# Kernel tuning notes

Measured on AMD Instinct MI355X. Metric: run time of the kernel, lower is better.

The kernel has to match this reference:

```python
import jax, jax.numpy as jnp
import numpy as np

B_, L, D_MODEL = 8, 2048, 512
EXPAND, D_STATE, HEADDIM, NGROUPS, D_CONV = 2, 16, 64, 1, 4
D_INNER = EXPAND * D_MODEL            # 1024
NHEADS = D_INNER // HEADDIM           # 16
CONV_DIM = D_INNER + 2 * NGROUPS * D_STATE   # 1056
D_IN_PROJ = 2 * D_INNER + 2 * NGROUPS * D_STATE + NHEADS  # 2096
EPS = 1e-5


def _mamba_params(key):
    ks = jax.random.split(key, 5)
    in_proj_w = jax.random.normal(ks[0], (D_IN_PROJ, D_MODEL), jnp.float32) * (D_MODEL ** -0.5)
    conv_w = jax.random.normal(ks[1], (CONV_DIM, 1, D_CONV), jnp.float32) * (D_CONV ** -0.5)
    conv_b = jnp.zeros((CONV_DIM,), jnp.float32)
    # inverse-softplus of dt ~ U[1e-3, 0.1] (mamba-ssm style init)
    dt_bias = jnp.log(jnp.expm1(jax.random.uniform(ks[2], (NHEADS,), jnp.float32, 1e-3, 0.1)))
    A_log = jnp.log(jax.random.uniform(ks[3], (NHEADS,), jnp.float32, 1.0, 16.0))
    Dp = jnp.ones((NHEADS,), jnp.float32)
    norm_w = jnp.ones((D_INNER,), jnp.float32)
    out_proj_w = jax.random.normal(ks[4], (D_MODEL, D_INNER), jnp.float32) * (D_INNER ** -0.5)
    return [in_proj_w, conv_w, conv_b, dt_bias, A_log, Dp, norm_w, out_proj_w]


def setup_inputs() -> dict:
    key = jax.random.key(0)
    k0, k1, k2 = jax.random.split(key, 3)
    d = {"x": jax.random.normal(k0, (B_, L, D_MODEL), jnp.float32)}
    names = ["in_proj_w", "conv_w", "conv_b", "dt_bias", "A_log", "Dp", "norm_w", "out_proj_w"]
    for pre, k in (("fwd_", k1), ("bwd_", k2)):
        for n, p in zip(names, _mamba_params(k)):
            d[pre + n] = p
    return d


def _silu(v):
    return v * jax.nn.sigmoid(v)


def _mamba2(u, in_proj_w, conv_w, conv_b, dt_bias, A_log, Dp, norm_w, out_proj_w):
    b, l, _ = u.shape
    zxbcdt = u @ in_proj_w.T                                # (b,l,D_IN_PROJ)
    z, xBC, dt = jnp.split(zxbcdt, [D_INNER, D_INNER + CONV_DIM], axis=-1)
    # causal depthwise conv1d + silu
    xc = jnp.transpose(xBC, (0, 2, 1))                      # (b,C,l)
    xc = jax.lax.conv_general_dilated(xc, conv_w, (1,), [(D_CONV - 1, 0)],
                                      feature_group_count=CONV_DIM)
    xBC = _silu(jnp.transpose(xc, (0, 2, 1)) + conv_b)      # (b,l,C)
    xs, Bm, Cm = jnp.split(xBC, [D_INNER, D_INNER + NGROUPS * D_STATE], axis=-1)
    xs = xs.reshape(b, l, NHEADS, HEADDIM)
    Bm = Bm.reshape(b, l, NGROUPS, D_STATE)[:, :, 0]        # ngroups=1 -> (b,l,N)
    Cm = Cm.reshape(b, l, NGROUPS, D_STATE)[:, :, 0]
    dt = jax.nn.softplus(dt + dt_bias)                      # (b,l,H)
    A = -jnp.exp(A_log)                                     # (H,)
    dA = jnp.exp(dt * A)                                    # (b,l,H), in (0,1)

    def step(h, inp):
        dA_t, dt_t, x_t, B_t, C_t = inp
        h = h * dA_t[:, :, None, None] + jnp.einsum('bh,bhp,bn->bhpn', dt_t, x_t, B_t)
        y = jnp.einsum('bhpn,bn->bhp', h, C_t)
        return h, y

    h0 = jnp.zeros((b, NHEADS, HEADDIM, D_STATE), u.dtype)
    seq = (jnp.moveaxis(dA, 1, 0), jnp.moveaxis(dt, 1, 0), jnp.moveaxis(xs, 1, 0),
           jnp.moveaxis(Bm, 1, 0), jnp.moveaxis(Cm, 1, 0))
    _, ys = jax.lax.scan(step, h0, seq)
    y = jnp.moveaxis(ys, 0, 1) + xs * Dp[None, None, :, None]   # (b,l,H,P)
    y = y.reshape(b, l, D_INNER)
    # RMSNormGated (norm_before_gate=False): rmsnorm(y * silu(z)) * w
    y = y * _silu(z)
    y = y * jax.lax.rsqrt(jnp.mean(y * y, axis=-1, keepdims=True) + EPS) * norm_w
    return y @ out_proj_w.T


def reference(x,
              fwd_in_proj_w, fwd_conv_w, fwd_conv_b, fwd_dt_bias, fwd_A_log, fwd_Dp, fwd_norm_w, fwd_out_proj_w,
              bwd_in_proj_w, bwd_conv_w, bwd_conv_b, bwd_dt_bias, bwd_A_log, bwd_Dp, bwd_norm_w, bwd_out_proj_w):
    fwd = _mamba2(x, fwd_in_proj_w, fwd_conv_w, fwd_conv_b, fwd_dt_bias, fwd_A_log, fwd_Dp, fwd_norm_w, fwd_out_proj_w)
    bwd = _mamba2(x[:, ::-1], bwd_in_proj_w, bwd_conv_w, bwd_conv_b, bwd_dt_bias, bwd_A_log, bwd_Dp, bwd_norm_w, bwd_out_proj_w)
    return fwd + bwd[:, ::-1]
```

## Files before the change

kernel.cpp:

```cpp
#include <hip/hip_runtime.h>
#include <stdint.h>

#define L_SEQ   2048
#define BATCH   8
#define DMODEL  512
#define DINNER  1024
#define NHEADS  16
#define HEADDIM 64
#define DSTATE  16
#define CONVDIM 1056
#define DINPROJ 2096
#define NPROJ   4192
#define NPROJ_P 4224
#define NROWS   (BATCH*L_SEQ)
#define NCH     32
#define CHLEN   64
#define XBCW    1072

typedef __attribute__((ext_vector_type(8))) short short8;
typedef __attribute__((ext_vector_type(4))) float f32x4;

static __device__ __forceinline__ unsigned short f2bf(float f) {
    unsigned int u = __float_as_uint(f);
    u += 0x7FFF + ((u >> 16) & 1);
    return (unsigned short)(u >> 16);
}
static __device__ __forceinline__ float bf2f(unsigned short u) {
    return __uint_as_float((unsigned int)u << 16);
}
static __device__ __forceinline__ float silu(float v) {
    return v / (1.f + __expf(-v));
}
static __device__ __forceinline__ void glds16(const unsigned short* g, unsigned short* l) {
    __builtin_amdgcn_global_load_lds(
        (const __attribute__((address_space(1))) unsigned int*)g,
        (__attribute__((address_space(3))) unsigned int*)l, 16, 0, 0);
}

#define PREP_N1 (NROWS*DMODEL)
#define PREP_N2 (NPROJ_P*DMODEL)
#define PREP_N3 (512*2048)
#define PREP_T  ((PREP_N1+PREP_N2+PREP_N3)/4)
static __device__ __forceinline__ uint2 pack4(float4 v) {
    uint2 o;
    o.x = (unsigned int)f2bf(v.x) | ((unsigned int)f2bf(v.y) << 16);
    o.y = (unsigned int)f2bf(v.z) | ((unsigned int)f2bf(v.w) << 16);
    return o;
}
__global__ void k_prep(const float* __restrict__ x,
                       const float* __restrict__ fwi, const float* __restrict__ bwi,
                       const float* __restrict__ fow, const float* __restrict__ bow,
                       unsigned short* __restrict__ XB, unsigned short* __restrict__ W1,
                       unsigned short* __restrict__ W2) {
    int i = blockIdx.x * 256 + threadIdx.x;
    if (i >= PREP_T) return;
    int j4 = i * 4;
    if (j4 < PREP_N1) {
        *(uint2*)&XB[j4] = pack4(*(const float4*)&x[j4]);
    } else if (j4 < PREP_N1 + PREP_N2) {
        int j = j4 - PREP_N1;
        const int FS = DINPROJ * DMODEL;
        uint2 o = {0u, 0u};
        if (j < 2 * FS)
            o = pack4(j < FS ? *(const float4*)&fwi[j] : *(const float4*)&bwi[j - FS]);
        *(uint2*)&W1[j] = o;
    } else {
        int j = j4 - PREP_N1 - PREP_N2;
        int n = j >> 11, k = j & 2047;
        const float* s = (k < DINNER) ? &fow[n * DINNER + k] : &bow[n * DINNER + k - DINNER];
        *(uint2*)&W2[j] = pack4(*(const float4*)s);
    }
}

#define BM 128
#define BN 128
#define BK 32

#define GEMM_BODY(NROUNDS, EPILOGUE)                                                        \
    __shared__ __align__(16) unsigned short as[2][BM][BK];                                  \
    __shared__ __align__(16) unsigned short bs[2][BN][BK];                                  \
    const int tid = threadIdx.x;                                                            \
    const int lane = tid & 63;                                                              \
    const int wave = tid >> 6;                                                              \
    const int wm = (wave & 1) * 64;                                                         \
    const int wn = (wave >> 1) * 64;                                                        \
    const int l16 = lane & 15;                                                              \
    const int q = lane >> 4;                                                                \
    const int sr = wave * 32;                                                               \
    const int lr = lane >> 2;                                                               \
    const int lc = (lane & 3) * 8;                                                          \
    f32x4 acc[4][4];                                                                        \
    for (int i = 0; i < 4; i++)                                                             \
        for (int j = 0; j < 4; j++) acc[i][j] = (f32x4){0.f, 0.f, 0.f, 0.f};                \
    const unsigned short* Ab = A + (size_t)(bm + sr + lr) * K + koff + lc;                  \
    const unsigned short* Bb = Bw + (size_t)(bn + sr + lr) * K + koff + lc;                 \
    glds16(Ab, &as[0][sr][0]);                                                              \
    glds16(Ab + (size_t)16 * K, &as[0][sr + 16][0]);                                        \
    glds16(Bb, &bs[0][sr][0]);                                                              \
    glds16(Bb + (size_t)16 * K, &bs[0][sr + 16][0]);                                        \
    __syncthreads();                                                                        \
    for (int r = 0; r < NROUNDS; r++) {                                                     \
        const int pb = r & 1;                                                               \
        if (r + 1 < NROUNDS) {               \
            const int kb = (r + 1) * BK;                                                    \
            glds16(Ab + kb, &as[pb ^ 1][sr][0]);                                            \
            glds16(Ab + (size_t)16 * K + kb, &as[pb ^ 1][sr + 16][0]);                      \
            glds16(Bb + kb, &bs[pb ^ 1][sr][0]);                                            \
            glds16(Bb + (size_t)16 * K + kb, &bs[pb ^ 1][sr + 16][0]);                      \
        }                                                                                   \
        short8 af[4], bfr[4];                                                               \
        for (int i = 0; i < 4; i++) af[i] = *(const short8*)&as[pb][wm + i * 16 + l16][q * 8]; \
        for (int j = 0; j < 4; j++) bfr[j] = *(const short8*)&bs[pb][wn + j * 16 + l16][q * 8]; \
        for (int i = 0; i < 4; i++)                                                         \
            for (int j = 0; j < 4; j++)                                                     \
                acc[i][j] = __builtin_amdgcn_mfma_f32_16x16x32_bf16(af[i], bfr[j], acc[i][j], 0, 0, 0); \
        __syncthreads();                          \
    }                                                                                       \
    EPILOGUE

#define GEMM_BODY_OUT(NROUNDS, EPILOGUE)                                                    \
    __shared__ __align__(16) unsigned short as[2][64][BK];                                  \
    __shared__ __align__(16) unsigned short bs[2][BN][BK];                                  \
    const int tid = threadIdx.x;                                                            \
    const int lane = tid & 63;                                                              \
    const int wave = tid >> 6;                                                              \
    const int wm = (wave & 1) * 32;                                                         \
    const int wn = (wave >> 1) * 64;                                                        \
    const int l16 = lane & 15;                                                              \
    const int q = lane >> 4;                                                                \
    const int sra = wave * 16;                                                              \
    const int srb = wave * 32;                                                              \
    const int lr = lane >> 2;                                                               \
    const int lc = (lane & 3) * 8;                                                          \
    f32x4 acc[2][4];                                                                        \
    for (int i = 0; i < 2; i++)                                                             \
        for (int j = 0; j < 4; j++) acc[i][j] = (f32x4){0.f, 0.f, 0.f, 0.f};                \
    const unsigned short* Ab = A + (size_t)(bm + sra + lr) * K + koff + lc;                 \
    const unsigned short* Bb = Bw + (size_t)(bn + srb + lr) * K + koff + lc;                \
    glds16(Ab, &as[0][sra][0]);                                                             \
    glds16(Bb, &bs[0][srb][0]);                                                             \
    glds16(Bb + (size_t)16 * K, &bs[0][srb + 16][0]);                                       \
    __syncthreads();                                                                        \
    for (int r = 0; r < NROUNDS; r++) {                                                     \
        const int pb = r & 1;                                                               \
        if (r + 1 < NROUNDS) {                                                              \
            const int kb = (r + 1) * BK;                                                    \
            glds16(Ab + kb, &as[pb ^ 1][sra][0]);                                           \
            glds16(Bb + kb, &bs[pb ^ 1][srb][0]);                                           \
            glds16(Bb + (size_t)16 * K + kb, &bs[pb ^ 1][srb + 16][0]);                     \
        }                                                                                   \
        short8 af[2], bfr[4];                                                               \
        for (int i = 0; i < 2; i++) af[i] = *(const short8*)&as[pb][wm + i * 16 + l16][q * 8]; \
        for (int j = 0; j < 4; j++) bfr[j] = *(const short8*)&bs[pb][wn + j * 16 + l16][q * 8]; \
        for (int i = 0; i < 2; i++)                                                         \
            for (int j = 0; j < 4; j++)                                                     \
                acc[i][j] = __builtin_amdgcn_mfma_f32_16x16x32_bf16(af[i], bfr[j], acc[i][j], 0, 0, 0); \
        __syncthreads();                                                                    \
    }                                                                                       \
    EPILOGUE

__global__ __launch_bounds__(256, 4) void k_gemm_proj(const unsigned short* __restrict__ A,
                                                      const unsigned short* __restrict__ Bw,
                                                      unsigned short* __restrict__ ZG,
                                                      unsigned short* __restrict__ XBCDT) {
    const int K = DMODEL;
    const int N = NPROJ;
    const int lin = blockIdx.x;
    const int xcd = lin & 7;
    const int idx = lin >> 3;
    const int mloc = idx & 15;
    const int n_tile = idx >> 4;
    const int bm = (mloc * 8 + xcd) * BM;
    const int bn = n_tile * BN;
    const int koff = 0;
    GEMM_BODY(16, {
        for (int i = 0; i < 4; i++) {
            int row0 = bm + wm + i * 16 + q * 4;
            for (int j = 0; j < 4; j++) {
                int col = bn + wn + j * 16 + l16;
                if (col < N) {
                    int dir = col >= DINPROJ;
                    int cc = col - dir * DINPROJ;
                    for (int r = 0; r < 4; r++) {
                        unsigned short v = f2bf(acc[i][j][r]);
                        size_t rowo = (size_t)(dir * NROWS + row0 + r);
                        if (cc < DINNER)
                            ZG[rowo * DINNER + cc] = v;
                        else
                            XBCDT[rowo * XBCW + (cc - DINNER)] = v;
                    }
                }
            }
        }
    })
}

__global__ __launch_bounds__(256) void k_gemm_out(const unsigned short* __restrict__ A,
                                                  const unsigned short* __restrict__ Bw,
                                                  float* __restrict__ C) {
    const int K = 2048;
    const int lin = blockIdx.x;
    const int xcd = lin & 7;
    const int idx = lin >> 3;
    const int mloc = idx & 31;
    const int n_tile = idx >> 5;
    const int bm = (mloc * 8 + xcd) * 64;
    const int bn = n_tile * BN;
    const int koff = 0;
    GEMM_BODY_OUT(64, {
        for (int i = 0; i < 2; i++) {
            int row0 = bm + wm + i * 16 + q * 4;
            for (int j = 0; j < 4; j++) {
                int col = bn + wn + j * 16 + l16;
                for (int r = 0; r < 4; r++)
                    C[(size_t)(row0 + r) * 512 + col] = acc[i][j][r];
            }
        }
    })
}

__global__ __launch_bounds__(256) void k_conv2(const unsigned short* __restrict__ XBCDT,
                                               const float* __restrict__ fw_w, const float* __restrict__ fw_b,
                                               const float* __restrict__ bw_w, const float* __restrict__ bw_b,
                                               unsigned short* __restrict__ XS, float* __restrict__ BCb) {
    __shared__ unsigned short sm[70][256];
    int t = threadIdx.x;
    int bidx = blockIdx.x;
    int lcn = bidx & 31;
    int b   = (bidx >> 5) & 7;
    int dir = (bidx >> 8) & 1;
    int ct  = bidx >> 9;
    int c0 = ct * 256;
    int l0 = lcn * 64;
    int c = c0 + t;
    const unsigned short* src = XBCDT + (size_t)dir * NROWS * XBCW;
    {
        const int rr = t >> 5;
        const int ch = t & 31;
        const int cc0 = c0 + ch * 8;
        const bool cok16 = (cc0 + 8 <= XBCW);
        const short8 z8 = {0, 0, 0, 0, 0, 0, 0, 0};
#pragma unroll
        for (int pass = 0; pass < 9; ++pass) {
            int r = pass * 8 + rr;
            if (r < 70) {
                int li = l0 - 3 + r;
                short8 v = z8;
                if (li >= 0 && li < L_SEQ && cok16)
                    v = *(const short8*)&src[(size_t)((b << 11) + li) * XBCW + cc0];
                *(short8*)&sm[r][ch * 8] = v;
            }
        }
    }
    __syncthreads();
    if (c >= CONVDIM) return;
    const float* w = (dir ? bw_w : fw_w) + c * 4;
    float bias = (dir ? bw_b : fw_b)[c];
    float wr[4];
    if (dir) { wr[0] = w[3]; wr[1] = w[2]; wr[2] = w[1]; wr[3] = w[0]; }
    else     { wr[0] = w[0]; wr[1] = w[1]; wr[2] = w[2]; wr[3] = w[3]; }
    int o = dir ? 3 : 0;
    float w0 = bf2f(sm[o][t]), w1 = bf2f(sm[o + 1][t]), w2 = bf2f(sm[o + 2][t]);
    unsigned short* xso = XS + (size_t)dir * NROWS * DINNER;
    float* bco = BCb + (size_t)dir * NROWS * 32;
    int rowbase = (b << 11) + l0;
#pragma unroll 4
    for (int l = 0; l < 64; l++) {
        float w3 = bf2f(sm[l + o + 3][t]);
        float acc = ((wr[0] * w0 + wr[1] * w1) + (wr[2] * w2 + wr[3] * w3)) + bias;
        float v = silu(acc);
        int row = rowbase + l;
        if (c < DINNER)
            xso[(size_t)row * DINNER + c] = f2bf(v);
        else
            bco[(size_t)row * 32 + (c - DINNER)] = v;
        w0 = w1; w1 = w2; w2 = w3;
    }
}

__global__ void k_dt(const unsigned short* __restrict__ XBCDT,
                     const float* __restrict__ fdtb, const float* __restrict__ fAl,
                     const float* __restrict__ bdtb, const float* __restrict__ bAl,
                     float* __restrict__ DT, float* __restrict__ DA) {
    int gid = blockIdx.x * 256 + threadIdx.x;
    if (gid >= 2 * NROWS * NHEADS) return;
    int h = gid & 15;
    int row = (gid >> 4) & (NROWS - 1);
    int dir = gid >> 18;
    float dtb = (dir ? bdtb : fdtb)[h];
    float Al = (dir ? bAl : fAl)[h];
    float x = bf2f(XBCDT[(size_t)(dir * NROWS + row) * XBCW + CONVDIM + h]) + dtb;
    float dt = (x > 15.f) ? x : log1pf(__expf(x));
    float dA = __expf(-__expf(Al) * dt);
    DT[gid] = dt;
    DA[gid] = dA;
}

__global__ __launch_bounds__(64) void k_scan_state(const unsigned short* __restrict__ XS,
                                                   const float* __restrict__ BCb,
                                                   const float* __restrict__ DT,
                                                   const float* __restrict__ DA,
                                                   float* __restrict__ S, float* __restrict__ P) {
    int idx = blockIdx.x;
    int c = idx & 31, hp = (idx >> 5) & 7, b = (idx >> 8) & 7, dir = idx >> 11;
    int t = threadIdx.x;
    int h = hp * 2 + (t >> 5);
    int p0 = (t & 31) * 2;
    const unsigned short* xs = XS + (size_t)dir * NROWS * DINNER;
    const float* bc = BCb + (size_t)dir * NROWS * 32;
    const float* dtp = DT + (size_t)dir * NROWS * NHEADS;
    const float* dap = DA + (size_t)dir * NROWS * NHEADS;
    float hreg0[16], hreg1[16];
#pragma unroll
    for (int n = 0; n < 16; n++) { hreg0[n] = 0.f; hreg1[n] = 0.f; }
    float Pp = 1.f;
#pragma unroll 4
    for (int tl = 0; tl < CHLEN; ++tl) {
        int tt = c * CHLEN + tl;
        int l = dir ? (L_SEQ - 1 - tt) : tt;
        int row = (b << 11) + l;
        unsigned int xv2 = *(const unsigned int*)&xs[(size_t)row * DINNER + h * HEADDIM + p0];
        float xv0 = bf2f((unsigned short)(xv2 & 0xffff));
        float xv1 = bf2f((unsigned short)(xv2 >> 16));
        float dt = dtp[row * 16 + h];
        float dA = dap[row * 16 + h];
        f32x4 Bv[4];
#pragma unroll
        for (int qq = 0; qq < 4; qq++) Bv[qq] = *(const f32x4*)&bc[(size_t)row * 32 + qq * 4];
        float k0 = dt * xv0, k1 = dt * xv1;
#pragma unroll
        for (int n = 0; n < 16; n++) {
            float bv = Bv[n >> 2][n & 3];
            hreg0[n] = fmaf(hreg0[n], dA, k0 * bv);
            hreg1[n] = fmaf(hreg1[n], dA, k1 * bv);
        }
        Pp *= dA;
    }
    int sh = (((dir * 8 + b) * 16 + h) * NCH + c);
#pragma unroll
    for (int qq = 0; qq < 4; qq++) {
        f32x4 v0 = {hreg0[qq * 4], hreg0[qq * 4 + 1], hreg0[qq * 4 + 2], hreg0[qq * 4 + 3]};
        f32x4 v1 = {hreg1[qq * 4], hreg1[qq * 4 + 1], hreg1[qq * 4 + 2], hreg1[qq * 4 + 3]};
        *(f32x4*)&S[(size_t)sh * 1024 + p0 * 16 + qq * 4] = v0;
        *(f32x4*)&S[(size_t)sh * 1024 + (p0 + 1) * 16 + qq * 4] = v1;
    }
    if ((t & 31) == 0) P[sh] = Pp;
}

__global__ void k_combine(float* __restrict__ S, const float* __restrict__ P,
                          float* __restrict__ SSQ) {
    int gid = blockIdx.x * 256 + threadIdx.x;
    if (gid < 2 * NROWS) SSQ[gid] = 0.f;
    if (gid >= 2 * 8 * 16 * 1024) return;
    int pn = gid & 1023;
    int base = gid >> 10;
    float H = 0.f;
#pragma unroll 4
    for (int c = 0; c < NCH; c++) {
        size_t o = ((size_t)base * NCH + c) * 1024 + pn;
        float s = S[o];
        S[o] = H;
        H = H * P[base * NCH + c] + s;
    }
}

__global__ __launch_bounds__(64) void k_scan_out(const unsigned short* __restrict__ XS,
                                                 const float* __restrict__ BCb,
                                                 const float* __restrict__ DT,
                                                 const float* __restrict__ DA,
                                                 const float* __restrict__ Hinit,
                                                 const float* __restrict__ fDp,
                                                 const float* __restrict__ bDp,
                                                 const unsigned short* __restrict__ ZG,
                                                 float* __restrict__ SSQ,
                                                 unsigned short* __restrict__ Y) {
    int idx = blockIdx.x;
    int c = idx & 31, hp = (idx >> 5) & 7, b = (idx >> 8) & 7, dir = idx >> 11;
    int t = threadIdx.x;
    int h = hp * 2 + (t >> 5);
    int p0 = (t & 31) * 2;
    const unsigned short* xs = XS + (size_t)dir * NROWS * DINNER;
    const unsigned short* zgd = ZG + (size_t)dir * NROWS * DINNER;
    const float* bc = BCb + (size_t)dir * NROWS * 32;
    const float* dtp = DT + (size_t)dir * NROWS * NHEADS;
    const float* dap = DA + (size_t)dir * NROWS * NHEADS;
    unsigned short* yo = Y + (size_t)dir * NROWS * DINNER;
    float* ssqd = SSQ + (size_t)dir * NROWS;
    float Dpv = (dir ? bDp : fDp)[h];
    int sh = (((dir * 8 + b) * 16 + h) * NCH + c);
    float hreg0[16], hreg1[16];
#pragma unroll
    for (int qq = 0; qq < 4; qq++) {
        f32x4 v0 = *(const f32x4*)&Hinit[(size_t)sh * 1024 + p0 * 16 + qq * 4];
        f32x4 v1 = *(const f32x4*)&Hinit[(size_t)sh * 1024 + (p0 + 1) * 16 + qq * 4];
#pragma unroll
        for (int e = 0; e < 4; e++) { hreg0[qq * 4 + e] = v0[e]; hreg1[qq * 4 + e] = v1[e]; }
    }
#pragma unroll 4
    for (int tl = 0; tl < CHLEN; ++tl) {
        int tt = c * CHLEN + tl;
        int l = dir ? (L_SEQ - 1 - tt) : tt;
        int row = (b << 11) + l;
        unsigned int xv2 = *(const unsigned int*)&xs[(size_t)row * DINNER + h * HEADDIM + p0];
        float xv0 = bf2f((unsigned short)(xv2 & 0xffff));
        float xv1 = bf2f((unsigned short)(xv2 >> 16));
        float dt = dtp[row * 16 + h];
        float dA = dap[row * 16 + h];
        f32x4 Bv[4], Cv[4];
#pragma unroll
        for (int qq = 0; qq < 4; qq++) Bv[qq] = *(const f32x4*)&bc[(size_t)row * 32 + qq * 4];
#pragma unroll
        for (int qq = 0; qq < 4; qq++) Cv[qq] = *(const f32x4*)&bc[(size_t)row * 32 + 16 + qq * 4];
        float k0 = dt * xv0, k1 = dt * xv1;
        float y0 = 0.f, y1 = 0.f;
#pragma unroll
        for (int n = 0; n < 16; n++) {
            float bv = Bv[n >> 2][n & 3];
            float cv = Cv[n >> 2][n & 3];
            hreg0[n] = fmaf(hreg0[n], dA, k0 * bv);
            hreg1[n] = fmaf(hreg1[n], dA, k1 * bv);
            y0 = fmaf(hreg0[n], cv, y0);
            y1 = fmaf(hreg1[n], cv, y1);
        }
        unsigned int zz = *(const unsigned int*)&zgd[(size_t)row * DINNER + h * HEADDIM + p0];
        float v0 = (y0 + xv0 * Dpv) * silu(bf2f((unsigned short)(zz & 0xffff)));
        float v1 = (y1 + xv1 * Dpv) * silu(bf2f((unsigned short)(zz >> 16)));
        unsigned int yw = (unsigned int)f2bf(v0) | ((unsigned int)f2bf(v1) << 16);
        *(unsigned int*)&yo[(size_t)row * DINNER + h * HEADDIM + p0] = yw;
        float pr = v0 * v0 + v1 * v1;
#pragma unroll
        for (int off = 16; off > 0; off >>= 1) pr += __shfl_down(pr, off);
        if ((t & 31) == 0) atomicAdd(&ssqd[row], pr);
    }
}

__global__ __launch_bounds__(256) void k_gatenorm(const unsigned short* __restrict__ Y,
                                                  const float* __restrict__ SSQ,
                                                  const float* __restrict__ fnw,
                                                  const float* __restrict__ bnw,
                                                  unsigned short* __restrict__ NRM) {
    int bid = blockIdx.x;
    int t = threadIdx.x;
    int sub = t >> 7;
    int tt = t & 127;
    int rid = bid * 2 + sub;
    int dir = rid >> 14;
    int row = rid & (NROWS - 1);
    int c = tt * 8;
    const size_t base = (size_t)rid * DINNER + c;
    uint4 yu = *(const uint4*)&Y[base];
    float scale = rsqrtf(SSQ[rid] * (1.f / 1024.f) + 1e-5f);
    const float* nw = (dir ? bnw : fnw) + c;
    f32x4 nw0 = *(const f32x4*)&nw[0];
    f32x4 nw1 = *(const f32x4*)&nw[4];
    const unsigned int yw[4] = {yu.x, yu.y, yu.z, yu.w};
    unsigned int ow[4];
#pragma unroll
    for (int e = 0; e < 4; e++) {
        float a = bf2f((unsigned short)(yw[e] & 0xffff)) * scale
                * (e < 2 ? nw0[e * 2]     : nw1[(e - 2) * 2]);
        float b = bf2f((unsigned short)(yw[e] >> 16)) * scale
                * (e < 2 ? nw0[e * 2 + 1] : nw1[(e - 2) * 2 + 1]);
        ow[e] = (unsigned int)f2bf(a) | ((unsigned int)f2bf(b) << 16);
    }
    uint4 o = {ow[0], ow[1], ow[2], ow[3]};
    *(uint4*)&NRM[(size_t)row * 2048 + dir * DINNER + c] = o;
}

extern "C" void kernel_launch(void* const* d_in, const int* in_sizes, int n_in,
                              void* d_out, int out_size, void* d_ws, size_t ws_size,
                              hipStream_t stream) {
    const float* x     = (const float*)d_in[0];
    const float* f_inw = (const float*)d_in[1];
    const float* f_cw  = (const float*)d_in[2];
    const float* f_cb  = (const float*)d_in[3];
    const float* f_dtb = (const float*)d_in[4];
    const float* f_Al  = (const float*)d_in[5];
    const float* f_Dp  = (const float*)d_in[6];
    const float* f_nw  = (const float*)d_in[7];
    const float* f_ow  = (const float*)d_in[8];
    const float* b_inw = (const float*)d_in[9];
    const float* b_cw  = (const float*)d_in[10];
    const float* b_cb  = (const float*)d_in[11];
    const float* b_dtb = (const float*)d_in[12];
    const float* b_Al  = (const float*)d_in[13];
    const float* b_Dp  = (const float*)d_in[14];
    const float* b_nw  = (const float*)d_in[15];
    const float* b_ow  = (const float*)d_in[16];

    char* ws = (char*)d_ws;
    size_t off = 0;
    auto alloc = [&](size_t bytes) {
        void* p = ws + off;
        off += (bytes + 255) & ~(size_t)255;
        return p;
    };
    unsigned short* XBCDT = (unsigned short*)alloc((size_t)2 * NROWS * XBCW * 2);
    unsigned short* NRM   = XBCDT;
    float* S = (float*)XBCDT;
    float* P = (float*)((char*)XBCDT + (size_t)2 * 8 * 16 * NCH * 1024 * 4);
    unsigned short* XS    = (unsigned short*)alloc((size_t)2 * NROWS * DINNER * 2);
    unsigned short* Yb    = XS;
    unsigned short* ZG    = (unsigned short*)alloc((size_t)2 * NROWS * DINNER * 2);
    unsigned short* W2    = (unsigned short*)alloc((size_t)512 * 2048 * 2);
    float* BCb  = (float*)alloc((size_t)2 * NROWS * 32 * 4);
    float* DT   = (float*)alloc((size_t)2 * NROWS * NHEADS * 4);
    float* DA   = (float*)alloc((size_t)2 * NROWS * NHEADS * 4);
    float* SSQ  = (float*)alloc((size_t)2 * NROWS * 4);
    char* unionBase = (char*)alloc((size_t)16777216 + (size_t)NPROJ_P * DMODEL * 2);
    unsigned short* XB = (unsigned short*)unionBase;
    unsigned short* W1 = (unsigned short*)(unionBase + 16777216);

    if (ws_size < off) return;

    k_prep<<<(PREP_T + 255) / 256, 256, 0, stream>>>(x, f_inw, b_inw, f_ow, b_ow, XB, W1, W2);
    k_gemm_proj<<<8 * 16 * 33, 256, 0, stream>>>(XB, W1, ZG, XBCDT);
    k_conv2<<<5 * 2 * 8 * 32, 256, 0, stream>>>(XBCDT, f_cw, f_cb, b_cw, b_cb, XS, BCb);
    {
        int n = 2 * NROWS * NHEADS;
        k_dt<<<(n + 255) / 256, 256, 0, stream>>>(XBCDT, f_dtb, f_Al, b_dtb, b_Al, DT, DA);
    }
    k_scan_state<<<2 * 8 * 8 * NCH, 64, 0, stream>>>(XS, BCb, DT, DA, S, P);
    {
        int n = 2 * 8 * 16 * 1024;
        k_combine<<<(n + 255) / 256, 256, 0, stream>>>(S, P, SSQ);
    }
    k_scan_out<<<2 * 8 * 8 * NCH, 64, 0, stream>>>(XS, BCb, DT, DA, S, f_Dp, b_Dp, ZG, SSQ, Yb);
    k_gatenorm<<<NROWS, 256, 0, stream>>>(Yb, SSQ, f_nw, b_nw, NRM);
    k_gemm_out<<<8 * 32 * 4, 256, 0, stream>>>(NRM, W2, (float*)d_out);
}
```

Before: 479.5 us.

## Fuse gated RMSNorm into output GEMM via weight folding and epilogue scaling

Removes the separate gate-norm kernel. The norm weight is folded into the bf16 output projection weights during prep, and the per-row rsqrt scale is applied in the GEMM epilogue. Forward and backward halves go into separate accumulators so each can take its own row scale. This saves a full read and write pass over the normalized activation buffer, at the cost of extra accumulator registers in the output GEMM and a slightly different rounding order.

```diff
diff --git a/kernel.cpp b/kernel.cpp
--- a/kernel.cpp
+++ b/kernel.cpp
@@ -50,6 +50,7 @@
 __global__ void k_prep(const float* __restrict__ x,
                        const float* __restrict__ fwi, const float* __restrict__ bwi,
                        const float* __restrict__ fow, const float* __restrict__ bow,
+                       const float* __restrict__ fnw, const float* __restrict__ bnw,
                        unsigned short* __restrict__ XB, unsigned short* __restrict__ W1,
                        unsigned short* __restrict__ W2) {
     int i = blockIdx.x * 256 + threadIdx.x;
@@ -67,8 +68,12 @@
     } else {
         int j = j4 - PREP_N1 - PREP_N2;
         int n = j >> 11, k = j & 2047;
-        const float* s = (k < DINNER) ? &fow[n * DINNER + k] : &bow[n * DINNER + k - DINNER];
-        *(uint2*)&W2[j] = pack4(*(const float4*)s);
+        float4 wv = (k < DINNER) ? *(const float4*)&fow[n * DINNER + k]
+                                 : *(const float4*)&bow[n * DINNER + k - DINNER];
+        float4 nv = (k < DINNER) ? *(const float4*)&fnw[k]
+                                 : *(const float4*)&bnw[k - DINNER];
+        wv.x *= nv.x; wv.y *= nv.y; wv.z *= nv.z; wv.w *= nv.w;
+        *(uint2*)&W2[j] = pack4(wv);
     }
 }
 
@@ -118,47 +123,6 @@
     }                                                                                       \
     EPILOGUE
 
-#define GEMM_BODY_OUT(NROUNDS, EPILOGUE)                                                    \
-    __shared__ __align__(16) unsigned short as[2][64][BK];                                  \
-    __shared__ __align__(16) unsigned short bs[2][BN][BK];                                  \
-    const int tid = threadIdx.x;                                                            \
-    const int lane = tid & 63;                                                              \
-    const int wave = tid >> 6;                                                              \
-    const int wm = (wave & 1) * 32;                                                         \
-    const int wn = (wave >> 1) * 64;                                                        \
-    const int l16 = lane & 15;                                                              \
-    const int q = lane >> 4;                                                                \
-    const int sra = wave * 16;                                                              \
-    const int srb = wave * 32;                                                              \
-    const int lr = lane >> 2;                                                               \
-    const int lc = (lane & 3) * 8;                                                          \
-    f32x4 acc[2][4];                                                                        \
-    for (int i = 0; i < 2; i++)                                                             \
-        for (int j = 0; j < 4; j++) acc[i][j] = (f32x4){0.f, 0.f, 0.f, 0.f};                \
-    const unsigned short* Ab = A + (size_t)(bm + sra + lr) * K + koff + lc;                 \
-    const unsigned short* Bb = Bw + (size_t)(bn + srb + lr) * K + koff + lc;                \
-    glds16(Ab, &as[0][sra][0]);                                                             \
-    glds16(Bb, &bs[0][srb][0]);                                                             \
-    glds16(Bb + (size_t)16 * K, &bs[0][srb + 16][0]);                                       \
-    __syncthreads();                                                                        \
-    for (int r = 0; r < NROUNDS; r++) {                                                     \
-        const int pb = r & 1;                                                               \
-        if (r + 1 < NROUNDS) {                                                              \
-            const int kb = (r + 1) * BK;                                                    \
-            glds16(Ab + kb, &as[pb ^ 1][sra][0]);                                           \
-            glds16(Bb + kb, &bs[pb ^ 1][srb][0]);                                           \
-            glds16(Bb + (size_t)16 * K + kb, &bs[pb ^ 1][srb + 16][0]);                     \
-        }                                                                                   \
-        short8 af[2], bfr[4];                                                               \
-        for (int i = 0; i < 2; i++) af[i] = *(const short8*)&as[pb][wm + i * 16 + l16][q * 8]; \
-        for (int j = 0; j < 4; j++) bfr[j] = *(const short8*)&bs[pb][wn + j * 16 + l16][q * 8]; \
-        for (int i = 0; i < 2; i++)                                                         \
-            for (int j = 0; j < 4; j++)                                                     \
-                acc[i][j] = __builtin_amdgcn_mfma_f32_16x16x32_bf16(af[i], bfr[j], acc[i][j], 0, 0, 0); \
-        __syncthreads();                                                                    \
-    }                                                                                       \
-    EPILOGUE
-
 __global__ __launch_bounds__(256, 4) void k_gemm_proj(const unsigned short* __restrict__ A,
                                                       const unsigned short* __restrict__ Bw,
                                                       unsigned short* __restrict__ ZG,
@@ -195,10 +159,12 @@
     })
 }
 
-__global__ __launch_bounds__(256) void k_gemm_out(const unsigned short* __restrict__ A,
+__global__ __launch_bounds__(256) void k_gemm_out(const unsigned short* __restrict__ Y,
                                                   const unsigned short* __restrict__ Bw,
+                                                  const float* __restrict__ SSQ,
                                                   float* __restrict__ C) {
-    const int K = 2048;
+    __shared__ __align__(16) unsigned short as[2][64][BK];
+    __shared__ __align__(16) unsigned short bs[2][BN][BK];
     const int lin = blockIdx.x;
     const int xcd = lin & 7;
     const int idx = lin >> 3;
@@ -206,17 +172,67 @@
     const int n_tile = idx >> 5;
     const int bm = (mloc * 8 + xcd) * 64;
     const int bn = n_tile * BN;
-    const int koff = 0;
-    GEMM_BODY_OUT(64, {
-        for (int i = 0; i < 2; i++) {
-            int row0 = bm + wm + i * 16 + q * 4;
+    const int tid = threadIdx.x;
+    const int lane = tid & 63;
+    const int wave = tid >> 6;
+    const int wm = (wave & 1) * 32;
+    const int wn = (wave >> 1) * 64;
+    const int l16 = lane & 15;
+    const int q = lane >> 4;
+    const int sra = wave * 16;
+    const int srb = wave * 32;
+    const int lr = lane >> 2;
+    const int lc = (lane & 3) * 8;
+    f32x4 accA[2][4], accF[2][4];
+    for (int i = 0; i < 2; i++)
+        for (int j = 0; j < 4; j++) {
+            accA[i][j] = (f32x4){0.f, 0.f, 0.f, 0.f};
+            accF[i][j] = (f32x4){0.f, 0.f, 0.f, 0.f};
+        }
+    const unsigned short* AF = Y + (size_t)(bm + sra + lr) * DINNER + lc;
+    const unsigned short* AB = AF + (size_t)NROWS * DINNER;
+    const unsigned short* Bb = Bw + (size_t)(bn + srb + lr) * 2048 + lc;
+    glds16(AF, &as[0][sra][0]);
+    glds16(Bb, &bs[0][srb][0]);
+    glds16(Bb + (size_t)16 * 2048, &bs[0][srb + 16][0]);
+    __syncthreads();
+    for (int r = 0; r < 64; r++) {
+        const int pb = r & 1;
+        if (r + 1 < 64) {
+            const int t = r + 1;
+            const unsigned short* asrc = (t < 32) ? AF + t * BK : AB + (t - 32) * BK;
+            const int kb = t * BK;
+            glds16(asrc, &as[pb ^ 1][sra][0]);
+            glds16(Bb + kb, &bs[pb ^ 1][srb][0]);
+            glds16(Bb + (size_t)16 * 2048 + kb, &bs[pb ^ 1][srb + 16][0]);
+        }
+        if (r == 32) {
+            for (int i = 0; i < 2; i++)
+                for (int j = 0; j < 4; j++) {
+                    accF[i][j] = accA[i][j];
+                    accA[i][j] = (f32x4){0.f, 0.f, 0.f, 0.f};
+                }
+        }
+        short8 af[2], bfr[4];
+        for (int i = 0; i < 2; i++) af[i] = *(const short8*)&as[pb][wm + i * 16 + l16][q * 8];
+        for (int j = 0; j < 4; j++) bfr[j] = *(const short8*)&bs[pb][wn + j * 16 + l16][q * 8];
+        for (int i = 0; i < 2; i++)
+            for (int j = 0; j < 4; j++)
+                accA[i][j] = __builtin_amdgcn_mfma_f32_16x16x32_bf16(af[i], bfr[j], accA[i][j], 0, 0, 0);
+        __syncthreads();
+    }
+    for (int i = 0; i < 2; i++) {
+        int row0 = bm + wm + i * 16 + q * 4;
+        for (int r = 0; r < 4; r++) {
+            int row = row0 + r;
+            float sf = rsqrtf(SSQ[row] * (1.f / 1024.f) + 1e-5f);
+            float sb = rsqrtf(SSQ[NROWS + row] * (1.f / 1024.f) + 1e-5f);
             for (int j = 0; j < 4; j++) {
                 int col = bn + wn + j * 16 + l16;
-                for (int r = 0; r < 4; r++)
-                    C[(size_t)(row0 + r) * 512 + col] = acc[i][j][r];
+                C[(size_t)row * 512 + col] = sf * accF[i][j][r] + sb * accA[i][j][r];
             }
         }
-    })
+    }
 }
 
 __global__ __launch_bounds__(256) void k_conv2(const unsigned short* __restrict__ XBCDT,
@@ -434,39 +450,6 @@
     }
 }
 
-__global__ __launch_bounds__(256) void k_gatenorm(const unsigned short* __restrict__ Y,
-                                                  const float* __restrict__ SSQ,
-                                                  const float* __restrict__ fnw,
-                                                  const float* __restrict__ bnw,
-                                                  unsigned short* __restrict__ NRM) {
-    int bid = blockIdx.x;
-    int t = threadIdx.x;
-    int sub = t >> 7;
-    int tt = t & 127;
-    int rid = bid * 2 + sub;
-    int dir = rid >> 14;
-    int row = rid & (NROWS - 1);
-    int c = tt * 8;
-    const size_t base = (size_t)rid * DINNER + c;
-    uint4 yu = *(const uint4*)&Y[base];
-    float scale = rsqrtf(SSQ[rid] * (1.f / 1024.f) + 1e-5f);
-    const float* nw = (dir ? bnw : fnw) + c;
-    f32x4 nw0 = *(const f32x4*)&nw[0];
-    f32x4 nw1 = *(const f32x4*)&nw[4];
-    const unsigned int yw[4] = {yu.x, yu.y, yu.z, yu.w};
-    unsigned int ow[4];
-#pragma unroll
-    for (int e = 0; e < 4; e++) {
-        float a = bf2f((unsigned short)(yw[e] & 0xffff)) * scale
-                * (e < 2 ? nw0[e * 2]     : nw1[(e - 2) * 2]);
-        float b = bf2f((unsigned short)(yw[e] >> 16)) * scale
-                * (e < 2 ? nw0[e * 2 + 1] : nw1[(e - 2) * 2 + 1]);
-        ow[e] = (unsigned int)f2bf(a) | ((unsigned int)f2bf(b) << 16);
-    }
-    uint4 o = {ow[0], ow[1], ow[2], ow[3]};
-    *(uint4*)&NRM[(size_t)row * 2048 + dir * DINNER + c] = o;
-}
-
 extern "C" void kernel_launch(void* const* d_in, const int* in_sizes, int n_in,
                               void* d_out, int out_size, void* d_ws, size_t ws_size,
                               hipStream_t stream) {
@@ -496,7 +479,6 @@
         return p;
     };
     unsigned short* XBCDT = (unsigned short*)alloc((size_t)2 * NROWS * XBCW * 2);
-    unsigned short* NRM   = XBCDT;
     float* S = (float*)XBCDT;
     float* P = (float*)((char*)XBCDT + (size_t)2 * 8 * 16 * NCH * 1024 * 4);
     unsigned short* XS    = (unsigned short*)alloc((size_t)2 * NROWS * DINNER * 2);
@@ -513,7 +495,8 @@
 
     if (ws_size < off) return;
 
-    k_prep<<<(PREP_T + 255) / 256, 256, 0, stream>>>(x, f_inw, b_inw, f_ow, b_ow, XB, W1, W2);
+    k_prep<<<(PREP_T + 255) / 256, 256, 0, stream>>>(x, f_inw, b_inw, f_ow, b_ow,
+                                                     f_nw, b_nw, XB, W1, W2);
     k_gemm_proj<<<8 * 16 * 33, 256, 0, stream>>>(XB, W1, ZG, XBCDT);
     k_conv2<<<5 * 2 * 8 * 32, 256, 0, stream>>>(XBCDT, f_cw, f_cb, b_cw, b_cb, XS, BCb);
     {
@@ -526,6 +509,5 @@
         k_combine<<<(n + 255) / 256, 256, 0, stream>>>(S, P, SSQ);
     }
     k_scan_out<<<2 * 8 * 8 * NCH, 64, 0, stream>>>(XS, BCb, DT, DA, S, f_Dp, b_Dp, ZG, SSQ, Yb);
-    k_gatenorm<<<NROWS, 256, 0, stream>>>(Yb, SSQ, f_nw, b_nw, NRM);
-    k_gemm_out<<<8 * 32 * 4, 256, 0, stream>>>(NRM, W2, (float*)d_out);
-}
+    k_gemm_out<<<8 * 32 * 4, 256, 0, stream>>>(Yb, W2, SSQ, (float*)d_out);
+}
```

Result: no change. 483.2 us (+0.8%).

## Move gating and RMS sum-of-squares from scan into gatenorm block reduction

Applied to the files above, without the earlier changes.

The scan output kernel no longer reads the z gate, applies silu, or does per-row atomicAdd of squared values. It now writes the ungated y directly. The gatenorm kernel loads y and z, applies the gate, and computes the row sum of squares with a wave shuffle plus a shared-memory reduction. This removes atomic contention and the SSQ buffer and its zeroing, at the cost of an extra z read in gatenorm and one more bf16 rounding before gating.

```diff
diff --git a/kernel.cpp b/kernel.cpp
--- a/kernel.cpp
+++ b/kernel.cpp
@@ -347,10 +347,8 @@
     if ((t & 31) == 0) P[sh] = Pp;
 }
 
-__global__ void k_combine(float* __restrict__ S, const float* __restrict__ P,
-                          float* __restrict__ SSQ) {
+__global__ void k_combine(float* __restrict__ S, const float* __restrict__ P) {
     int gid = blockIdx.x * 256 + threadIdx.x;
-    if (gid < 2 * NROWS) SSQ[gid] = 0.f;
     if (gid >= 2 * 8 * 16 * 1024) return;
     int pn = gid & 1023;
     int base = gid >> 10;
@@ -371,8 +369,6 @@
                                                  const float* __restrict__ Hinit,
                                                  const float* __restrict__ fDp,
                                                  const float* __restrict__ bDp,
-                                                 const unsigned short* __restrict__ ZG,
-                                                 float* __restrict__ SSQ,
                                                  unsigned short* __restrict__ Y) {
     int idx = blockIdx.x;
     int c = idx & 31, hp = (idx >> 5) & 7, b = (idx >> 8) & 7, dir = idx >> 11;
@@ -380,12 +376,10 @@
     int h = hp * 2 + (t >> 5);
     int p0 = (t & 31) * 2;
     const unsigned short* xs = XS + (size_t)dir * NROWS * DINNER;
-    const unsigned short* zgd = ZG + (size_t)dir * NROWS * DINNER;
     const float* bc = BCb + (size_t)dir * NROWS * 32;
     const float* dtp = DT + (size_t)dir * NROWS * NHEADS;
     const float* dap = DA + (size_t)dir * NROWS * NHEADS;
     unsigned short* yo = Y + (size_t)dir * NROWS * DINNER;
-    float* ssqd = SSQ + (size_t)dir * NROWS;
     float Dpv = (dir ? bDp : fDp)[h];
     int sh = (((dir * 8 + b) * 16 + h) * NCH + c);
     float hreg0[16], hreg1[16];
@@ -422,20 +416,14 @@
             y0 = fmaf(hreg0[n], cv, y0);
             y1 = fmaf(hreg1[n], cv, y1);
         }
-        unsigned int zz = *(const unsigned int*)&zgd[(size_t)row * DINNER + h * HEADDIM + p0];
-        float v0 = (y0 + xv0 * Dpv) * silu(bf2f((unsigned short)(zz & 0xffff)));
-        float v1 = (y1 + xv1 * Dpv) * silu(bf2f((unsigned short)(zz >> 16)));
-        unsigned int yw = (unsigned int)f2bf(v0) | ((unsigned int)f2bf(v1) << 16);
+        unsigned int yw = (unsigned int)f2bf(y0 + xv0 * Dpv)
+                        | ((unsigned int)f2bf(y1 + xv1 * Dpv) << 16);
         *(unsigned int*)&yo[(size_t)row * DINNER + h * HEADDIM + p0] = yw;
-        float pr = v0 * v0 + v1 * v1;
-#pragma unroll
-        for (int off = 16; off > 0; off >>= 1) pr += __shfl_down(pr, off);
-        if ((t & 31) == 0) atomicAdd(&ssqd[row], pr);
     }
 }
 
 __global__ __launch_bounds__(256) void k_gatenorm(const unsigned short* __restrict__ Y,
-                                                  const float* __restrict__ SSQ,
+                                                  const unsigned short* __restrict__ ZG,
                                                   const float* __restrict__ fnw,
                                                   const float* __restrict__ bnw,
                                                   unsigned short* __restrict__ NRM) {
@@ -447,20 +435,37 @@
     int dir = rid >> 14;
     int row = rid & (NROWS - 1);
     int c = tt * 8;
-    const size_t base = (size_t)rid * DINNER + c;
+    const size_t base = (size_t)(dir * NROWS + row) * DINNER + c;
     uint4 yu = *(const uint4*)&Y[base];
-    float scale = rsqrtf(SSQ[rid] * (1.f / 1024.f) + 1e-5f);
+    uint4 zu = *(const uint4*)&ZG[base];
+    float v[8];
+    {
+        const unsigned int yw[4] = {yu.x, yu.y, yu.z, yu.w};
+        const unsigned int zw[4] = {zu.x, zu.y, zu.z, zu.w};
+#pragma unroll
+        for (int e = 0; e < 4; e++) {
+            v[e * 2]     = bf2f((unsigned short)(yw[e] & 0xffff)) * silu(bf2f((unsigned short)(zw[e] & 0xffff)));
+            v[e * 2 + 1] = bf2f((unsigned short)(yw[e] >> 16))    * silu(bf2f((unsigned short)(zw[e] >> 16)));
+        }
+    }
+    float ss = 0.f;
+#pragma unroll
+    for (int e = 0; e < 8; e++) ss += v[e] * v[e];
+#pragma unroll
+    for (int off = 32; off > 0; off >>= 1) ss += __shfl_down(ss, off);
+    __shared__ float red[4];
+    if ((t & 63) == 0) red[t >> 6] = ss;
+    __syncthreads();
+    float tot = red[sub * 2] + red[sub * 2 + 1];
+    float scale = rsqrtf(tot * (1.f / 1024.f) + 1e-5f);
     const float* nw = (dir ? bnw : fnw) + c;
     f32x4 nw0 = *(const f32x4*)&nw[0];
     f32x4 nw1 = *(const f32x4*)&nw[4];
-    const unsigned int yw[4] = {yu.x, yu.y, yu.z, yu.w};
     unsigned int ow[4];
 #pragma unroll
     for (int e = 0; e < 4; e++) {
-        float a = bf2f((unsigned short)(yw[e] & 0xffff)) * scale
-                * (e < 2 ? nw0[e * 2]     : nw1[(e - 2) * 2]);
-        float b = bf2f((unsigned short)(yw[e] >> 16)) * scale
-                * (e < 2 ? nw0[e * 2 + 1] : nw1[(e - 2) * 2 + 1]);
+        float a = v[e * 2]     * scale * (e < 2 ? nw0[e * 2]     : nw1[(e - 2) * 2]);
+        float b = v[e * 2 + 1] * scale * (e < 2 ? nw0[e * 2 + 1] : nw1[(e - 2) * 2 + 1]);
         ow[e] = (unsigned int)f2bf(a) | ((unsigned int)f2bf(b) << 16);
     }
     uint4 o = {ow[0], ow[1], ow[2], ow[3]};
@@ -506,7 +511,6 @@
     float* BCb  = (float*)alloc((size_t)2 * NROWS * 32 * 4);
     float* DT   = (float*)alloc((size_t)2 * NROWS * NHEADS * 4);
     float* DA   = (float*)alloc((size_t)2 * NROWS * NHEADS * 4);
-    float* SSQ  = (float*)alloc((size_t)2 * NROWS * 4);
     char* unionBase = (char*)alloc((size_t)16777216 + (size_t)NPROJ_P * DMODEL * 2);
     unsigned short* XB = (unsigned short*)unionBase;
     unsigned short* W1 = (unsigned short*)(unionBase + 16777216);
@@ -523,9 +527,9 @@
     k_scan_state<<<2 * 8 * 8 * NCH, 64, 0, stream>>>(XS, BCb, DT, DA, S, P);
     {
         int n = 2 * 8 * 16 * 1024;
-        k_combine<<<(n + 255) / 256, 256, 0, stream>>>(S, P, SSQ);
-    }
-    k_scan_out<<<2 * 8 * 8 * NCH, 64, 0, stream>>>(XS, BCb, DT, DA, S, f_Dp, b_Dp, ZG, SSQ, Yb);
-    k_gatenorm<<<NROWS, 256, 0, stream>>>(Yb, SSQ, f_nw, b_nw, NRM);
+        k_combine<<<(n + 255) / 256, 256, 0, stream>>>(S, P);
+    }
+    k_scan_out<<<2 * 8 * 8 * NCH, 64, 0, stream>>>(XS, BCb, DT, DA, S, f_Dp, b_Dp, Yb);
+    k_gatenorm<<<NROWS, 256, 0, stream>>>(Yb, ZG, f_nw, b_nw, NRM);
     k_gemm_out<<<8 * 32 * 4, 256, 0, stream>>>(NRM, W2, (float*)d_out);
 }
```

Result: faster. 458.5 us (-4.4%).
